# Optimization experiments

Hardware: AMD Instinct MI355X
Metric: run time of the kernel (lower is better)

The kernel has to match this reference:

```python
import jax, jax.numpy as jnp
import numpy as np


def setup_inputs() -> dict:
    key = jax.random.key(0)
    ks = jax.random.split(key, 7)
    B, C, H, W = 16, 256, 1, 4096
    x = jax.random.normal(ks[0], (B, C, H, W), dtype=jnp.float32)
    init = lambda k, s: jax.random.normal(k, s, dtype=jnp.float32) * 0.02
    return {
        "x": x,
        "Wq": init(ks[1], (C, C)), "bq": jnp.zeros((C,), jnp.float32),
        "Wk": init(ks[2], (C, C)), "bk": jnp.zeros((C,), jnp.float32),
        "Wv": init(ks[3], (C, C)), "bv": jnp.zeros((C,), jnp.float32),
    }


def reference(x, Wq, bq, Wk, bk, Wv, bv):
    B, C, H, W = x.shape
    xs = jnp.transpose(x[:, :, 0, :], (0, 2, 1))  # [B, W, C]
    Q = xs @ Wq.T + bq  # [B, W, C]
    K = xs @ Wk.T + bk
    V = xs @ Wv.T + bv
    scale = jnp.sqrt(jnp.asarray(C, dtype=Q.dtype))

    # radius-1 sliding window along width; pad so window gather is static
    Kp = jnp.pad(K, ((0, 0), (1, 1), (0, 0)))  # [B, W+2, C]
    Vp = jnp.pad(V, ((0, 0), (1, 1), (0, 0)))
    idx = jnp.arange(W)[:, None] + jnp.arange(3)[None, :]  # padded indices [W,3]
    pos = idx - 1  # original positions (may be -1 or W -> invalid at edges)
    valid = (pos >= 0) & (pos < W)  # [W, 3]

    Kw = Kp[:, idx]  # [B, W, 3, C]
    Vw = Vp[:, idx]  # [B, W, 3, C]

    scores = jnp.einsum('bwc,bwkc->bwk', Q, Kw) / scale  # [B, W, 3]
    scores = jnp.where(valid[None], scores, jnp.asarray(-1e9, scores.dtype))
    attn = jax.nn.softmax(scores, axis=-1)
    out = jnp.einsum('bwk,bwkc->bwc', attn, Vw)  # [B, W, C]
    # [B, W, C] -> [B, C, 1, W]
    return jnp.transpose(out, (0, 2, 1))[:, :, None, :]
```

## Files before the change

kernel.cpp:

```cpp
#include <hip/hip_runtime.h>
#include <hip/hip_bf16.h>

#define C_DIM 256
#define W_DIM 4096
#define LDS_BYTES 162528

typedef unsigned short u16;
typedef short s16x8 __attribute__((ext_vector_type(8)));
typedef unsigned short u16x8 __attribute__((ext_vector_type(8)));
typedef unsigned short u16x4 __attribute__((ext_vector_type(4)));
typedef float f32x16 __attribute__((ext_vector_type(16)));

__device__ __forceinline__ u16 f2b(float f) {
  return __builtin_bit_cast(u16, __float2bfloat16(f));
}
__device__ __forceinline__ float b2f(u16 u) {
  return __builtin_bit_cast(float, ((unsigned)u) << 16);
}

__global__ __launch_bounds__(256) void prep_kernel(
    const float* __restrict__ Wq, const float* __restrict__ bq,
    const float* __restrict__ Wk, const float* __restrict__ bk,
    const float* __restrict__ Wv, char* __restrict__ ws) {
  u16* Mb   = (u16*)ws;
  u16* Wvb  = (u16*)(ws + 131072);
  float* u0 = (float*)(ws + 262144);
  float* u1 = (float*)(ws + 263168);
  float* c0p = (float*)(ws + 264192);
  int bid = blockIdx.x, t = threadIdx.x;
  if (bid < 256) {
    __shared__ float Wqs[256*17];
    __shared__ float Wks[256*17];
    int i0 = (bid >> 4) << 4, j0 = (bid & 15) << 4;
    for (int it = 0; it < 16; ++it) {
      int e = t + 256*it; int a = e >> 4, ii = e & 15;
      Wqs[a*17+ii] = Wq[a*256 + i0 + ii];
      Wks[a*17+ii] = Wk[a*256 + j0 + ii];
    }
    __syncthreads();
    int ii = t >> 4, jj = t & 15;
    float acc = 0.f;
    #pragma unroll 8
    for (int a = 0; a < 256; ++a) acc += Wqs[a*17+ii] * Wks[a*17+jj];
    Mb[(i0+ii)*256 + j0 + jj] = f2b(acc);
  } else if (bid == 256) {
    int j = t;
    float a0 = 0.f, a1 = 0.f;
    #pragma unroll 4
    for (int a = 0; a < 256; ++a) {
      a0 += bq[a] * Wk[a*256 + j];
      a1 += bk[a] * Wq[a*256 + j];
    }
    u0[j] = a0; u1[j] = a1;
    __shared__ float red[256];
    red[t] = bq[t] * bk[t];
    __syncthreads();
    if (t == 0) { float s = 0.f; for (int a = 0; a < 256; ++a) s += red[a]; *c0p = s; }
  } else {
    int base = ((bid - 257)*256 + t) * 4;
    const float4 v = *reinterpret_cast<const float4*>(Wv + base);
    ushort4 pk = make_ushort4(f2b(v.x), f2b(v.y), f2b(v.z), f2b(v.w));
    *reinterpret_cast<ushort4*>(Wvb + base) = pk;
  }
}

__global__ __launch_bounds__(512, 2) void main_kernel(
    const float* __restrict__ x, const char* __restrict__ ws,
    const float* __restrict__ bv, float* __restrict__ out) {
  const u16* Mb   = (const u16*)ws;
  const u16* Wvb  = (const u16*)(ws + 131072);
  const float* u0g = (const float*)(ws + 262144);
  const float* u1g = (const float*)(ws + 263168);
  const float c0  = *(const float*)(ws + 264192);

  extern __shared__ char lds[];
  u16*   Xt  = (u16*)lds;
  float* Ps  = (float*)(lds + 132608);
  float* ABs = (float*)(lds + 157376);
  float* fS  = (float*)(lds + 159440);
  float* U   = (float*)(lds + 159456);
  float* bvs = (float*)(lds + 161504);

  const int bid = blockIdx.x;
  const int t = threadIdx.x;
  const int wv = t >> 6, l = t & 63;
  const int col = l & 31, half = l >> 5;
  const int rs = wv & 3, cs = wv >> 2;

  const int b  = bid >> 4;
  const int cw = bid & 15;
  const int w0 = cw << 8;
  const float* xb = x + (size_t)b * (C_DIM*W_DIM);
  float* outb = out + (size_t)b * (C_DIM*W_DIM);

  if (t < 4) fS[t] = 0.f;
  if (t < 256) { U[t] = u0g[t]; U[256+t] = u1g[t]; bvs[t] = bv[t]; }
  __syncthreads();

  {
    #pragma unroll
    for (int p = 0; p < 4; ++p) {
      int j = 64*p + l;
      int w = w0 - 1 + j;
      bool ok = (w >= 0);
      const float* xp = xb + w;
      float xr[32];
      #pragma unroll
      for (int g = 0; g < 4; ++g)
        #pragma unroll
        for (int e = 0; e < 8; ++e)
          xr[g*8+e] = ok ? xp[(size_t)((4*wv+g)*8 + e) * W_DIM] : 0.f;
      float pa = 0.f, pb_ = 0.f;
      #pragma unroll
      for (int g = 0; g < 4; ++g) {
        int kk = 4*wv + g;
        union { u16 u[8]; u16x8 v; } pk;
        #pragma unroll
        for (int e = 0; e < 8; ++e) {
          float v = xr[g*8+e];
          pk.u[e] = f2b(v);
          pa  += U[kk*8+e] * v;
          pb_ += U[256 + kk*8+e] * v;
        }
        *reinterpret_cast<u16x8*>(Xt + (kk*259 + j)*8) = pk.v;
      }
      Ps[wv*258 + j] = pa;
      Ps[2064 + wv*258 + j] = pb_;
    }
    if (l < 3) {
      int j = 256 + l;
      int w = w0 - 1 + j;
      bool real = (l < 2) && (w < W_DIM);
      const float* xpe = xb + w;
      float pa = 0.f, pb_ = 0.f;
      #pragma unroll
      for (int g = 0; g < 4; ++g) {
        int kk = 4*wv + g;
        union { u16 u[8]; u16x8 v; } pk;
        #pragma unroll
        for (int e = 0; e < 8; ++e) {
          float v = real ? xpe[(size_t)(kk*8+e) * W_DIM] : 0.f;
          pk.u[e] = f2b(v);
          pa  += U[kk*8+e] * v;
          pb_ += U[256 + kk*8+e] * v;
        }
        *reinterpret_cast<u16x8*>(Xt + (kk*259 + j)*8) = pk.v;
      }
      if (l < 2) {
        Ps[wv*258 + j] = pa;
        Ps[2064 + wv*258 + j] = pb_;
      }
    }
  }
  __syncthreads();

  f32x16 acc0[4], acc1[4];
  #pragma unroll
  for (int ni = 0; ni < 4; ++ni)
    #pragma unroll
    for (int r = 0; r < 16; ++r) { acc0[ni][r] = 0.f; acc1[ni][r] = 0.f; }
  {
    const u16* Arow0 = Mb + (64*rs + col)*256 + 8*half;
    const u16* Arow1 = Arow0 + 32*256;
    #pragma unroll
    for (int kk = 0; kk < 16; ++kk) {
      s16x8 a0 = *reinterpret_cast<const s16x8*>(Arow0 + 16*kk);
      s16x8 a1 = *reinterpret_cast<const s16x8*>(Arow1 + 16*kk);
      const u16* Bb = Xt + (2*kk + half)*259*8;
      #pragma unroll
      for (int ni = 0; ni < 4; ++ni) {
        s16x8 bfr = *reinterpret_cast<const s16x8*>(Bb + (32*(4*cs+ni) + col)*8);
        acc0[ni] = __builtin_amdgcn_mfma_f32_32x32x16_bf16(a0, bfr, acc0[ni], 0, 0, 0);
        acc1[ni] = __builtin_amdgcn_mfma_f32_32x32x16_bf16(a1, bfr, acc1[ni], 0, 0, 0);
      }
    }
  }

  {
    int i = t >> 1, kq = t & 1;
    float xi255 = b2f(Xt[((i>>3)*259 + 255)*8 + (i&7)]);
    float xi256 = b2f(Xt[((i>>3)*259 + 256)*8 + (i&7)]);
    float a1 = 0.f, a2 = 0.f;
    const u16* Mrow = Mb + i*256 + 128*kq;
    #pragma unroll
    for (int kk8 = 0; kk8 < 16; ++kk8) {
      int sA = 16*kq + kk8;
      s16x8 m8 = *reinterpret_cast<const s16x8*>(Mrow + 8*kk8);
      u16x8 xk6 = *reinterpret_cast<const u16x8*>(Xt + (sA*259 + 256)*8);
      u16x8 xk7 = *reinterpret_cast<const u16x8*>(Xt + (sA*259 + 257)*8);
      #pragma unroll
      for (int e = 0; e < 8; ++e) {
        float m = b2f((u16)m8[e]);
        a1 += m * b2f(xk6[e]);
        a2 += m * b2f(xk7[e]);
      }
    }
    float p1 = xi256*a1, p2 = xi256*a2, p3 = xi255*a1;
    #pragma unroll
    for (int d = 1; d < 64; d <<= 1) {
      p1 += __shfl_xor(p1, d); p2 += __shfl_xor(p2, d); p3 += __shfl_xor(p3, d);
    }
    if (l == 0) { atomicAdd(&fS[0], p1); atomicAdd(&fS[1], p2); atomicAdd(&fS[2], p3); }
  }
  for (int i = t; i < 516; i += 512) {
    int which = (i >= 258) ? 1 : 0;
    int jj = i - 258*which;
    float s = 0.f;
    #pragma unroll
    for (int g = 0; g < 8; ++g) s += Ps[which*2064 + g*258 + jj];
    ABs[which*258 + jj] = s;
  }
  __syncthreads();

  {
    #pragma unroll
    for (int rt = 0; rt < 2; ++rt) {
      const int rg = 2*rs + rt;
      #pragma unroll
      for (int ni = 0; ni < 4; ++ni) {
        int jt = 32*(4*cs+ni) + col;
        int jm = (jt > 0) ? jt-1 : 0;
        int jp = jt + 1;
        float s0 = 0.f, s1 = 0.f, s2 = 0.f;
        #pragma unroll
        for (int q = 0; q < 4; ++q) {
          const u16* base = Xt + (4*rg + q)*259*8 + 4*half;
          u16x4 xm = *reinterpret_cast<const u16x4*>(base + jm*8);
          u16x4 xc = *reinterpret_cast<const u16x4*>(base + jt*8);
          u16x4 xp = *reinterpret_cast<const u16x4*>(base + jp*8);
          const f32x16& A = rt ? acc1[ni] : acc0[ni];
          #pragma unroll
          for (int r4 = 0; r4 < 4; ++r4) {
            float g0 = A[4*q + r4];
            s2 += g0 * b2f(xm[r4]);
            s1 += g0 * b2f(xc[r4]);
            s0 += g0 * b2f(xp[r4]);
          }
        }
        s0 += __shfl_xor(s0, 32);
        s1 += __shfl_xor(s1, 32);
        s2 += __shfl_xor(s2, 32);
        if (half == 0) {
          Ps[0*2064 + rg*258 + jt+1] = s0;
          if (jt >= 1) Ps[1*2064 + rg*258 + jt]   = s1;
          if (jt >= 2) Ps[2*2064 + rg*258 + jt-1] = s2;
        }
      }
    }
  }
  __syncthreads();

  {
    float aw0[4], aw1[4], aw2[4];
    #pragma unroll
    for (int p = 0; p < 4; ++p) {
      int oc = 64*p + l;
      int jp = oc + 1;
      float d0 = 0.f, d1 = 0.f, d2 = 0.f;
      #pragma unroll
      for (int g = 0; g < 8; ++g) {
        d0 += Ps[0*2064 + g*258 + jp];
        d1 += Ps[1*2064 + g*258 + jp];
        d2 += Ps[2*2064 + g*258 + jp];
      }
      if (oc == 255)      { d1 = fS[0]; d2 = fS[1]; }
      else if (oc == 254) { d2 = fS[2]; }
      float am = ABs[jp-1], ac_ = ABs[jp], ap_ = ABs[jp+1];
      float be = ABs[258 + jp];
      float sc0 = (d0 + am + be + c0) * 0.0625f;
      float sc1 = (d1 + ac_ + be + c0) * 0.0625f;
      float sc2 = (d2 + ap_ + be + c0) * 0.0625f;
      int w = w0 + oc;
      bool v0 = (w >= 1), v2 = (w + 1 < W_DIM);
      const float NEG = -1e30f;
      float m = fmaxf(v0 ? sc0 : NEG, fmaxf(sc1, v2 ? sc2 : NEG));
      float e0v = v0 ? __expf(sc0 - m) : 0.f;
      float e1v = __expf(sc1 - m);
      float e2v = v2 ? __expf(sc2 - m) : 0.f;
      float inv = 1.f / (e0v + e1v + e2v);
      aw0[p] = e0v*inv; aw1[p] = e1v*inv; aw2[p] = e2v*inv;
    }
    #pragma unroll
    for (int g = 0; g < 4; ++g) {
      u16* base = Xt + (4*wv + g)*259*8;
      u16x8 xrd[12];
      #pragma unroll
      for (int p = 0; p < 4; ++p)
        #pragma unroll
        for (int i = 0; i < 3; ++i)
          xrd[p*3+i] = *reinterpret_cast<const u16x8*>(base + (64*p + l + i)*8);
      __builtin_amdgcn_sched_barrier(0);
      #pragma unroll
      for (int p = 0; p < 4; ++p) {
        union { u16 u[8]; u16x8 v; } pk;
        #pragma unroll
        for (int e = 0; e < 8; ++e)
          pk.u[e] = f2b(aw0[p]*b2f(xrd[p*3][e]) + aw1[p]*b2f(xrd[p*3+1][e])
                        + aw2[p]*b2f(xrd[p*3+2][e]));
        *reinterpret_cast<u16x8*>(base + (64*p + l + 1)*8) = pk.v;
      }
      __builtin_amdgcn_sched_barrier(0);
    }
  }
  __syncthreads();

  {
    #pragma unroll
    for (int ni = 0; ni < 4; ++ni)
      #pragma unroll
      for (int r = 0; r < 16; ++r) { acc0[ni][r] = 0.f; acc1[ni][r] = 0.f; }
    const u16* Arow0 = Wvb + (64*rs + col)*256 + 8*half;
    const u16* Arow1 = Arow0 + 32*256;
    #pragma unroll
    for (int kk = 0; kk < 16; ++kk) {
      s16x8 a0 = *reinterpret_cast<const s16x8*>(Arow0 + 16*kk);
      s16x8 a1 = *reinterpret_cast<const s16x8*>(Arow1 + 16*kk);
      const u16* Bb = Xt + (2*kk + half)*259*8;
      #pragma unroll
      for (int ni = 0; ni < 4; ++ni) {
        s16x8 bfr = *reinterpret_cast<const s16x8*>(Bb + (1 + 32*(4*cs+ni) + col)*8);
        acc0[ni] = __builtin_amdgcn_mfma_f32_32x32x16_bf16(a0, bfr, acc0[ni], 0, 0, 0);
        acc1[ni] = __builtin_amdgcn_mfma_f32_32x32x16_bf16(a1, bfr, acc1[ni], 0, 0, 0);
      }
    }
    #pragma unroll
    for (int ni = 0; ni < 4; ++ni)
      #pragma unroll
      for (int r = 0; r < 16; ++r) {
        int rloc = (r&3) + 8*(r>>2) + 4*half;
        int crow0 = 64*rs + rloc;
        int crow1 = crow0 + 32;
        int oc = 32*(4*cs+ni) + col;
        outb[(size_t)crow0*W_DIM + w0 + oc] = acc0[ni][r] + bvs[crow0];
        outb[(size_t)crow1*W_DIM + w0 + oc] = acc1[ni][r] + bvs[crow1];
      }
  }
}

extern "C" void kernel_launch(void* const* d_in, const int* in_sizes, int n_in,
                              void* d_out, int out_size, void* d_ws, size_t ws_size,
                              hipStream_t stream) {
  (void)in_sizes; (void)n_in; (void)out_size; (void)ws_size;
  const float* x  = (const float*)d_in[0];
  const float* Wq = (const float*)d_in[1];
  const float* bq = (const float*)d_in[2];
  const float* Wk = (const float*)d_in[3];
  const float* bk = (const float*)d_in[4];
  const float* Wv = (const float*)d_in[5];
  const float* bv = (const float*)d_in[6];
  float* out = (float*)d_out;
  char* ws = (char*)d_ws;

  hipFuncSetAttribute((const void*)main_kernel,
                      hipFuncAttributeMaxDynamicSharedMemorySize, LDS_BYTES);
  prep_kernel<<<321, 256, 0, stream>>>(Wq, bq, Wk, bk, Wv, ws);
  main_kernel<<<256, 512, LDS_BYTES, stream>>>(x, ws, bv, out);
}
```

Baseline: 84.43 us.

## Split GEMM tiles per wave into two sequential column halves to halve accumulators

Each wave previously owned a 64-row by 128-column output tile, holding eight 32x32 MFMA accumulators. It now owns 32 rows by all 256 columns and processes them in two sequential halves of four accumulators each, for both the score GEMM and the V GEMM. This halves accumulator register pressure, which could allow higher occupancy or avoid spills. In exchange, each B fragment is reused by only one MFMA instead of two, so LDS B-fragment traffic per MFMA doubles.

```diff
diff --git a/kernel.cpp b/kernel.cpp
--- a/kernel.cpp
+++ b/kernel.cpp
@@ -85,7 +85,6 @@
   const int t = threadIdx.x;
   const int wv = t >> 6, l = t & 63;
   const int col = l & 31, half = l >> 5;
-  const int rs = wv & 3, cs = wv >> 2;
 
   const int b  = bid >> 4;
   const int cw = bid & 15;
@@ -154,24 +153,21 @@
   }
   __syncthreads();
 
-  f32x16 acc0[4], acc1[4];
+  f32x16 acc[4];
   #pragma unroll
   for (int ni = 0; ni < 4; ++ni)
     #pragma unroll
-    for (int r = 0; r < 16; ++r) { acc0[ni][r] = 0.f; acc1[ni][r] = 0.f; }
-  {
-    const u16* Arow0 = Mb + (64*rs + col)*256 + 8*half;
-    const u16* Arow1 = Arow0 + 32*256;
+    for (int r = 0; r < 16; ++r) acc[ni][r] = 0.f;
+  const u16* Arow1 = Mb + (32*wv + col)*256 + 8*half;
+  {
     #pragma unroll
     for (int kk = 0; kk < 16; ++kk) {
-      s16x8 a0 = *reinterpret_cast<const s16x8*>(Arow0 + 16*kk);
-      s16x8 a1 = *reinterpret_cast<const s16x8*>(Arow1 + 16*kk);
+      s16x8 a = *reinterpret_cast<const s16x8*>(Arow1 + 16*kk);
       const u16* Bb = Xt + (2*kk + half)*259*8;
       #pragma unroll
       for (int ni = 0; ni < 4; ++ni) {
-        s16x8 bfr = *reinterpret_cast<const s16x8*>(Bb + (32*(4*cs+ni) + col)*8);
-        acc0[ni] = __builtin_amdgcn_mfma_f32_32x32x16_bf16(a0, bfr, acc0[ni], 0, 0, 0);
-        acc1[ni] = __builtin_amdgcn_mfma_f32_32x32x16_bf16(a1, bfr, acc1[ni], 0, 0, 0);
+        s16x8 bfr = *reinterpret_cast<const s16x8*>(Bb + (32*ni + col)*8);
+        acc[ni] = __builtin_amdgcn_mfma_f32_32x32x16_bf16(a, bfr, acc[ni], 0, 0, 0);
       }
     }
   }
@@ -214,37 +210,80 @@
 
   {
     #pragma unroll
-    for (int rt = 0; rt < 2; ++rt) {
-      const int rg = 2*rs + rt;
+    for (int ni = 0; ni < 4; ++ni) {
+      int jt = 32*ni + col;
+      int jm = (jt > 0) ? jt-1 : 0;
+      int jp = jt + 1;
+      float s0 = 0.f, s1 = 0.f, s2 = 0.f;
+      #pragma unroll
+      for (int q = 0; q < 4; ++q) {
+        const u16* base = Xt + (4*wv + q)*259*8 + 4*half;
+        u16x4 xm = *reinterpret_cast<const u16x4*>(base + jm*8);
+        u16x4 xc = *reinterpret_cast<const u16x4*>(base + jt*8);
+        u16x4 xp = *reinterpret_cast<const u16x4*>(base + jp*8);
+        #pragma unroll
+        for (int r4 = 0; r4 < 4; ++r4) {
+          float g0 = acc[ni][4*q + r4];
+          s2 += g0 * b2f(xm[r4]);
+          s1 += g0 * b2f(xc[r4]);
+          s0 += g0 * b2f(xp[r4]);
+        }
+      }
+      s0 += __shfl_xor(s0, 32);
+      s1 += __shfl_xor(s1, 32);
+      s2 += __shfl_xor(s2, 32);
+      if (half == 0) {
+        Ps[0*2064 + wv*258 + jt+1] = s0;
+        if (jt >= 1) Ps[1*2064 + wv*258 + jt]   = s1;
+        if (jt >= 2) Ps[2*2064 + wv*258 + jt-1] = s2;
+      }
+    }
+  }
+
+  #pragma unroll
+  for (int ni = 0; ni < 4; ++ni)
+    #pragma unroll
+    for (int r = 0; r < 16; ++r) acc[ni][r] = 0.f;
+  {
+    #pragma unroll
+    for (int kk = 0; kk < 16; ++kk) {
+      s16x8 a = *reinterpret_cast<const s16x8*>(Arow1 + 16*kk);
+      const u16* Bb = Xt + (2*kk + half)*259*8;
       #pragma unroll
       for (int ni = 0; ni < 4; ++ni) {
-        int jt = 32*(4*cs+ni) + col;
-        int jm = (jt > 0) ? jt-1 : 0;
-        int jp = jt + 1;
-        float s0 = 0.f, s1 = 0.f, s2 = 0.f;
-        #pragma unroll
-        for (int q = 0; q < 4; ++q) {
-          const u16* base = Xt + (4*rg + q)*259*8 + 4*half;
-          u16x4 xm = *reinterpret_cast<const u16x4*>(base + jm*8);
-          u16x4 xc = *reinterpret_cast<const u16x4*>(base + jt*8);
-          u16x4 xp = *reinterpret_cast<const u16x4*>(base + jp*8);
-          const f32x16& A = rt ? acc1[ni] : acc0[ni];
-          #pragma unroll
-          for (int r4 = 0; r4 < 4; ++r4) {
-            float g0 = A[4*q + r4];
-            s2 += g0 * b2f(xm[r4]);
-            s1 += g0 * b2f(xc[r4]);
-            s0 += g0 * b2f(xp[r4]);
-          }
+        s16x8 bfr = *reinterpret_cast<const s16x8*>(Bb + (32*(ni+4) + col)*8);
+        acc[ni] = __builtin_amdgcn_mfma_f32_32x32x16_bf16(a, bfr, acc[ni], 0, 0, 0);
+      }
+    }
+  }
+  {
+    #pragma unroll
+    for (int ni = 0; ni < 4; ++ni) {
+      int jt = 32*(ni+4) + col;
+      int jm = jt-1;
+      int jp = jt + 1;
+      float s0 = 0.f, s1 = 0.f, s2 = 0.f;
+      #pragma unroll
+      for (int q = 0; q < 4; ++q) {
+        const u16* base = Xt + (4*wv + q)*259*8 + 4*half;
+        u16x4 xm = *reinterpret_cast<const u16x4*>(base + jm*8);
+        u16x4 xc = *reinterpret_cast<const u16x4*>(base + jt*8);
+        u16x4 xp = *reinterpret_cast<const u16x4*>(base + jp*8);
+        #pragma unroll
+        for (int r4 = 0; r4 < 4; ++r4) {
+          float g0 = acc[ni][4*q + r4];
+          s2 += g0 * b2f(xm[r4]);
+          s1 += g0 * b2f(xc[r4]);
+          s0 += g0 * b2f(xp[r4]);
         }
-        s0 += __shfl_xor(s0, 32);
-        s1 += __shfl_xor(s1, 32);
-        s2 += __shfl_xor(s2, 32);
-        if (half == 0) {
-          Ps[0*2064 + rg*258 + jt+1] = s0;
-          if (jt >= 1) Ps[1*2064 + rg*258 + jt]   = s1;
-          if (jt >= 2) Ps[2*2064 + rg*258 + jt-1] = s2;
-        }
+      }
+      s0 += __shfl_xor(s0, 32);
+      s1 += __shfl_xor(s1, 32);
+      s2 += __shfl_xor(s2, 32);
+      if (half == 0) {
+        Ps[0*2064 + wv*258 + jt+1] = s0;
+        Ps[1*2064 + wv*258 + jt]   = s1;
+        Ps[2*2064 + wv*258 + jt-1] = s2;
       }
     }
   }
@@ -304,35 +343,51 @@
   }
   __syncthreads();
 
-  {
+  const u16* Arow2 = Wvb + (32*wv + col)*256 + 8*half;
+  #pragma unroll
+  for (int ni = 0; ni < 4; ++ni)
+    #pragma unroll
+    for (int r = 0; r < 16; ++r) acc[ni][r] = 0.f;
+  {
+    #pragma unroll
+    for (int kk = 0; kk < 16; ++kk) {
+      s16x8 a = *reinterpret_cast<const s16x8*>(Arow2 + 16*kk);
+      const u16* Bb = Xt + (2*kk + half)*259*8;
+      #pragma unroll
+      for (int ni = 0; ni < 4; ++ni) {
+        s16x8 bfr = *reinterpret_cast<const s16x8*>(Bb + (1 + 32*ni + col)*8);
+        acc[ni] = __builtin_amdgcn_mfma_f32_32x32x16_bf16(a, bfr, acc[ni], 0, 0, 0);
+      }
+    }
     #pragma unroll
     for (int ni = 0; ni < 4; ++ni)
       #pragma unroll
-      for (int r = 0; r < 16; ++r) { acc0[ni][r] = 0.f; acc1[ni][r] = 0.f; }
-    const u16* Arow0 = Wvb + (64*rs + col)*256 + 8*half;
-    const u16* Arow1 = Arow0 + 32*256;
+      for (int r = 0; r < 16; ++r) {
+        int crow = 32*wv + (r&3) + 8*(r>>2) + 4*half;
+        outb[(size_t)crow*W_DIM + w0 + 32*ni + col] = acc[ni][r] + bvs[crow];
+      }
+  }
+  #pragma unroll
+  for (int ni = 0; ni < 4; ++ni)
+    #pragma unroll
+    for (int r = 0; r < 16; ++r) acc[ni][r] = 0.f;
+  {
     #pragma unroll
     for (int kk = 0; kk < 16; ++kk) {
-      s16x8 a0 = *reinterpret_cast<const s16x8*>(Arow0 + 16*kk);
-      s16x8 a1 = *reinterpret_cast<const s16x8*>(Arow1 + 16*kk);
+      s16x8 a = *reinterpret_cast<const s16x8*>(Arow2 + 16*kk);
       const u16* Bb = Xt + (2*kk + half)*259*8;
       #pragma unroll
       for (int ni = 0; ni < 4; ++ni) {
-        s16x8 bfr = *reinterpret_cast<const s16x8*>(Bb + (1 + 32*(4*cs+ni) + col)*8);
-        acc0[ni] = __builtin_amdgcn_mfma_f32_32x32x16_bf16(a0, bfr, acc0[ni], 0, 0, 0);
-        acc1[ni] = __builtin_amdgcn_mfma_f32_32x32x16_bf16(a1, bfr, acc1[ni], 0, 0, 0);
+        s16x8 bfr = *reinterpret_cast<const s16x8*>(Bb + (1 + 32*(ni+4) + col)*8);
+        acc[ni] = __builtin_amdgcn_mfma_f32_32x32x16_bf16(a, bfr, acc[ni], 0, 0, 0);
       }
     }
     #pragma unroll
     for (int ni = 0; ni < 4; ++ni)
       #pragma unroll
       for (int r = 0; r < 16; ++r) {
-        int rloc = (r&3) + 8*(r>>2) + 4*half;
-        int crow0 = 64*rs + rloc;
-        int crow1 = crow0 + 32;
-        int oc = 32*(4*cs+ni) + col;
-        outb[(size_t)crow0*W_DIM + w0 + oc] = acc0[ni][r] + bvs[crow0];
-        outb[(size_t)crow1*W_DIM + w0 + oc] = acc1[ni][r] + bvs[crow1];
+        int crow = 32*wv + (r&3) + 8*(r>>2) + 4*half;
+        outb[(size_t)crow*W_DIM + w0 + 32*(ni+4) + col] = acc[ni][r] + bvs[crow];
       }
   }
 }
```

Result: no change. 85.27 us (+1.0%).
